# Kernel tuning notes

Hardware: AMD Instinct MI355X
Metric: run time of the kernel (lower is better)

Reference implementation:

```python
import jax, jax.numpy as jnp
import numpy as np

NEG_SLOPE = 0.01  # nn.LeakyReLU default


def leaky_relu(x):
    return jnp.where(x >= 0, x, NEG_SLOPE * x)


def gcn_conv(x, W, b, src, dst, n_nodes):
    """PyG GCNConv: add self loops, symmetric D^-1/2 (A+I) D^-1/2 norm, then x @ W + b."""
    h = x @ W  # [N, D]
    # degree with self-loops (edge weight 1 each, +1 for the self loop)
    deg = jnp.zeros((n_nodes,), dtype=x.dtype).at[dst].add(1.0) + 1.0
    dinv = jax.lax.rsqrt(deg)  # deg >= 1 thanks to self loops
    norm = dinv[src] * dinv[dst]  # [E]
    msg = h[src] * norm[:, None]  # gather + scale, [E, D]
    agg = jnp.zeros_like(h).at[dst].add(msg)  # scatter-add over targets
    agg = agg + h * (dinv * dinv)[:, None]  # self-loop contribution
    return agg + b


def setup_inputs() -> dict:
    key = jax.random.key(0)
    ks = jax.random.split(key, 12)
    N, E = 100000, 640000
    ND, D, C = 239, 128, 2
    x = jax.random.normal(ks[0], (N, ND), dtype=jnp.float32)
    edge_index = jax.random.randint(ks[1], (2, E), 0, N, dtype=jnp.int64)
    edge_type = jax.random.randint(ks[2], (E,), 0, 4, dtype=jnp.int64)
    s = 0.05
    W_in = jax.random.normal(ks[3], (ND, D), dtype=jnp.float32) * s
    b_in = jax.random.normal(ks[4], (D,), dtype=jnp.float32) * s
    W_g = jax.random.normal(ks[5], (D, D), dtype=jnp.float32) * s
    b_g = jax.random.normal(ks[6], (D,), dtype=jnp.float32) * s
    W_o1 = jax.random.normal(ks[7], (D, D), dtype=jnp.float32) * s
    b_o1 = jax.random.normal(ks[8], (D,), dtype=jnp.float32) * s
    W_o2 = jax.random.normal(ks[9], (D, C), dtype=jnp.float32) * s
    b_o2 = jax.random.normal(ks[10], (C,), dtype=jnp.float32) * s
    return {"x": x, "edge_index": edge_index, "edge_type": edge_type,
            "W_in": W_in, "b_in": b_in, "W_g": W_g, "b_g": b_g,
            "W_o1": W_o1, "b_o1": b_o1, "W_o2": W_o2, "b_o2": b_o2}


def reference(x, edge_index, edge_type, W_in, b_in, W_g, b_g, W_o1, b_o1, W_o2, b_o2):
    n_nodes = x.shape[0]
    src, dst = edge_index[0], edge_index[1]
    h = leaky_relu(x @ W_in + b_in)
    h = gcn_conv(h, W_g, b_g, src, dst, n_nodes)
    # dropout is identity in eval mode (training=False)
    h = gcn_conv(h, W_g, b_g, src, dst, n_nodes)  # same shared GCNConv instance
    h = leaky_relu(h @ W_o1 + b_o1)
    return h @ W_o2 + b_o2
```

## Files before the change

### kernel.cpp

```cpp
#include <hip/hip_runtime.h>
#include <hip/hip_bf16.h>


typedef __attribute__((ext_vector_type(8))) __bf16 bf16x8;
typedef __attribute__((ext_vector_type(4))) float f32x4;

__global__ __launch_bounds__(256) void wtr_k(const float* __restrict__ W, ushort* __restrict__ Wt,
                                             int K, int Kp) {
  int idx = blockIdx.x * 256 + threadIdx.x;
  if (idx >= 128 * Kp) return;
  int n = idx / Kp, k = idx % Kp;
  float v = (k < K) ? W[(size_t)k * 128 + n] : 0.f;
  __hip_bfloat16 h = __float2bfloat16(v);
  Wt[idx] = *(ushort*)&h;
}


__global__ __launch_bounds__(256) void zero_k(int* __restrict__ p, int n) {
  int i = blockIdx.x * 256 + threadIdx.x;
  if (i < n) p[i] = 0;
}

__global__ __launch_bounds__(256) void hist_k(const int* __restrict__ dst, int* __restrict__ cnt, int E) {
  int e = blockIdx.x * 256 + threadIdx.x;
  if (e < E) atomicAdd(&cnt[dst[e]], 1);
}

__global__ __launch_bounds__(256) void dinv_k(const int* __restrict__ cnt, float* __restrict__ dinv, int N) {
  int i = blockIdx.x * 256 + threadIdx.x;
  if (i < N) dinv[i] = rsqrtf((float)cnt[i] + 1.0f);
}

__global__ __launch_bounds__(256) void scan1_k(const int* __restrict__ cnt, int* __restrict__ rp,
                                               int* __restrict__ bsum, int N) {
  __shared__ int sd[256];
  int t = threadIdx.x;
  int base = blockIdx.x * 1024 + t * 4;
  int v0 = (base + 0 < N) ? cnt[base + 0] : 0;
  int v1 = (base + 1 < N) ? cnt[base + 1] : 0;
  int v2 = (base + 2 < N) ? cnt[base + 2] : 0;
  int v3 = (base + 3 < N) ? cnt[base + 3] : 0;
  int ts = v0 + v1 + v2 + v3;
  sd[t] = ts;
  __syncthreads();
  for (int off = 1; off < 256; off <<= 1) {
    int y = (t >= off) ? sd[t - off] : 0;
    __syncthreads();
    sd[t] += y;
    __syncthreads();
  }
  int x = sd[t] - ts;
  if (t == 255) bsum[blockIdx.x] = sd[255];
  if (base + 0 < N) rp[base + 0] = x; x += v0;
  if (base + 1 < N) rp[base + 1] = x; x += v1;
  if (base + 2 < N) rp[base + 2] = x; x += v2;
  if (base + 3 < N) rp[base + 3] = x;
}

__global__ __launch_bounds__(256) void scan2_k(int* __restrict__ bsum, int NB) {
  __shared__ int sd[256];
  int t = threadIdx.x;
  int base = t * 4;
  int v0 = (base + 0 < NB) ? bsum[base + 0] : 0;
  int v1 = (base + 1 < NB) ? bsum[base + 1] : 0;
  int v2 = (base + 2 < NB) ? bsum[base + 2] : 0;
  int v3 = (base + 3 < NB) ? bsum[base + 3] : 0;
  int ts = v0 + v1 + v2 + v3;
  sd[t] = ts;
  __syncthreads();
  for (int off = 1; off < 256; off <<= 1) {
    int y = (t >= off) ? sd[t - off] : 0;
    __syncthreads();
    sd[t] += y;
    __syncthreads();
  }
  int x = sd[t] - ts;
  if (base + 0 < NB) bsum[base + 0] = x; x += v0;
  if (base + 1 < NB) bsum[base + 1] = x; x += v1;
  if (base + 2 < NB) bsum[base + 2] = x; x += v2;
  if (base + 3 < NB) bsum[base + 3] = x;
}

__global__ __launch_bounds__(256) void scan3_k(int* __restrict__ rp, int* __restrict__ pos,
                                               const int* __restrict__ bsum, int N, int E) {
  int i = blockIdx.x * 256 + threadIdx.x;
  if (i < N) {
    int v = rp[i] + bsum[i >> 10];
    rp[i] = v;
    pos[i] = v;
  }
  if (i == 0) rp[N] = E;
}

__global__ __launch_bounds__(256) void fill_k(const int* __restrict__ src, const int* __restrict__ dst,
                                              const float* __restrict__ dinv,
                                              int* __restrict__ pos, int2* __restrict__ ew, int E) {
  int e = blockIdx.x * 256 + threadIdx.x;
  if (e < E) {
    int d = dst[e];
    int s = src[e];
    int idx = atomicAdd(&pos[d], 1);
    ew[idx] = make_int2(s, __float_as_int(dinv[s] * dinv[d]));
  }
}


template <int MODE, int ASRC>
__global__ __launch_bounds__(512, 4) void mgemm_k(const void* __restrict__ Av,
                                                  const ushort* __restrict__ Wt,
                                                  const float* __restrict__ bias,
                                                  const float* __restrict__ W2,
                                                  const float* __restrict__ b2,
                                                  void* __restrict__ C, int N, int Kg, int Ka) {
  __shared__ uint4 Al[128 * 16];
  __shared__ uint4 Wl[128 * 16];
  const int tid = threadIdx.x;
  const int wave = tid >> 6;
  const int lane = tid & 63;
  const int l16 = lane & 15;
  const int quad = lane >> 4;
  const int m0 = blockIdx.x * 128;

  f32x4 acc[8] = {};

  const int r_s = tid >> 4;
  const int j8 = tid & 15;
  const int nch = Kg >> 7;

  for (int kc = 0; kc < nch; ++kc) {
    const int kbase = kc << 7;
    if (kc) __syncthreads();
#pragma unroll
    for (int it = 0; it < 4; ++it) {
      int m = it * 32 + r_s;
      uint4 v;
      if constexpr (ASRC == 0) {
        v = *(const uint4*)((const ushort*)Av + (size_t)(m0 + m) * Kg + kbase + j8 * 8);
      } else {
        int row = m0 + m;
        int rc = row < N ? row : N - 1;
        int c0 = kbase + j8 * 8;
        union { uint4 u; __hip_bfloat16 h[8]; } cv;
        if (c0 >= Ka) {
          cv.u = make_uint4(0, 0, 0, 0);
        } else {
          const float* xp = (const float*)Av;
          size_t s = (size_t)rc * Ka + c0;
          size_t base = s & ~(size_t)3;
          int ph = (int)(s & 3);
          size_t NT = (size_t)N * Ka;
          if (base + 12 <= NT) {
            const float4* bp = (const float4*)(xp + base);
            float4 f0 = bp[0], f1 = bp[1], f2 = bp[2];
            float w[12] = {f0.x, f0.y, f0.z, f0.w, f1.x, f1.y, f1.z, f1.w,
                           f2.x, f2.y, f2.z, f2.w};
#pragma unroll
            for (int j = 0; j < 8; ++j) {
              float f = ph == 0 ? w[j] : ph == 1 ? w[j + 1] : ph == 2 ? w[j + 2] : w[j + 3];
              cv.h[j] = __float2bfloat16(f);
            }
          } else {
#pragma unroll
            for (int j = 0; j < 8; ++j) {
              size_t idx = s + j;
              float f = (idx < NT && c0 + j < Ka) ? xp[idx] : 0.f;
              cv.h[j] = __float2bfloat16(f);
            }
          }
        }
        v = cv.u;
      }
      Al[m * 16 + (j8 ^ (m & 15))] = v;
    }
#pragma unroll
    for (int it = 0; it < 4; ++it) {
      int n = it * 32 + r_s;
      uint4 v = *(const uint4*)(Wt + (size_t)n * Kg + kbase + j8 * 8);
      Wl[n * 16 + (j8 ^ (n & 15))] = v;
    }
    __syncthreads();
#pragma unroll
    for (int s = 0; s < 4; ++s) {
      const int j = s * 4 + quad;
      const int swz = j ^ l16;
      bf16x8 a = *(const bf16x8*)&Al[(wave * 16 + l16) * 16 + swz];
#pragma unroll
      for (int c = 0; c < 8; ++c) {
        bf16x8 b = *(const bf16x8*)&Wl[(c * 16 + l16) * 16 + swz];
        acc[c] = __builtin_amdgcn_mfma_f32_16x16x32_bf16(a, b, acc[c], 0, 0, 0);
      }
    }
  }

  float bv[8];
#pragma unroll
  for (int c = 0; c < 8; ++c) bv[c] = bias[c * 16 + l16];

  if constexpr (MODE == 3) {
    float w20[8], w21[8];
#pragma unroll
    for (int c = 0; c < 8; ++c) {
      int colj = c * 16 + l16;
      w20[c] = W2[colj * 2 + 0];
      w21[c] = W2[colj * 2 + 1];
    }
    float bb0 = b2[0], bb1 = b2[1];
#pragma unroll
    for (int reg = 0; reg < 4; ++reg) {
      float o0 = 0.f, o1 = 0.f;
#pragma unroll
      for (int c = 0; c < 8; ++c) {
        float v = acc[c][reg] + bv[c];
        v = v >= 0.f ? v : 0.01f * v;
        o0 = fmaf(v, w20[c], o0);
        o1 = fmaf(v, w21[c], o1);
      }
      o0 += __shfl_xor(o0, 1); o0 += __shfl_xor(o0, 2);
      o0 += __shfl_xor(o0, 4); o0 += __shfl_xor(o0, 8);
      o1 += __shfl_xor(o1, 1); o1 += __shfl_xor(o1, 2);
      o1 += __shfl_xor(o1, 4); o1 += __shfl_xor(o1, 8);
      int row = m0 + wave * 16 + quad * 4 + reg;
      if (l16 == 0 && row < N)
        *(float2*)((float*)C + (size_t)row * 2) = make_float2(o0 + bb0, o1 + bb1);
    }
    return;
  }

#pragma unroll
  for (int reg = 0; reg < 4; ++reg) {
    int row = m0 + wave * 16 + quad * 4 + reg;
    if (row < N) {
#pragma unroll
      for (int c = 0; c < 8; ++c) {
        float v = acc[c][reg] + bv[c];
        if (MODE == 2) v = v >= 0.f ? v : 0.01f * v;
        __hip_bfloat16 h = __float2bfloat16(v);
        ((ushort*)C)[(size_t)row * 128 + c * 16 + l16] = *(ushort*)&h;
      }
    }
  }
}


__global__ __launch_bounds__(256) void agg_k(const ushort* __restrict__ T,
                                             const float* __restrict__ dinv,
                                             const int* __restrict__ rp,
                                             const int2* __restrict__ ew,
                                             ushort* __restrict__ O, int N) {
  int l = threadIdx.x & 15;
  int node = blockIdx.x * 16 + (threadIdx.x >> 4);
  if (node >= N) return;
  float di = dinv[node];
  float dsq = di * di;
  const uint4* T4 = (const uint4*)T;
  float a[8];
  {
    uint4 sv = T4[(size_t)node * 16 + l];
    uint u[4] = {sv.x, sv.y, sv.z, sv.w};
#pragma unroll
    for (int p = 0; p < 4; ++p) {
      a[2 * p + 0] = __uint_as_float(u[p] << 16) * dsq;
      a[2 * p + 1] = __uint_as_float(u[p] & 0xFFFF0000u) * dsq;
    }
  }
  int e1 = rp[node + 1];
  for (int e = rp[node]; e < e1; ++e) {
    int2 pw = ew[e];
    float w = __int_as_float(pw.y);
    uint4 v = T4[(size_t)pw.x * 16 + l];
    uint u[4] = {v.x, v.y, v.z, v.w};
#pragma unroll
    for (int p = 0; p < 4; ++p) {
      a[2 * p + 0] = fmaf(__uint_as_float(u[p] << 16), w, a[2 * p + 0]);
      a[2 * p + 1] = fmaf(__uint_as_float(u[p] & 0xFFFF0000u), w, a[2 * p + 1]);
    }
  }
  union { uint4 v; ushort s[8]; } uo;
#pragma unroll
  for (int j = 0; j < 8; ++j) {
    __hip_bfloat16 h = __float2bfloat16(a[j]);
    uo.s[j] = *(ushort*)&h;
  }
  ((uint4*)O)[(size_t)node * 16 + l] = uo.v;
}


extern "C" void kernel_launch(void* const* d_in, const int* in_sizes, int n_in,
                              void* d_out, int out_size, void* d_ws, size_t ws_size,
                              hipStream_t stream) {
  const float* x = (const float*)d_in[0];
  const int* ei = (const int*)d_in[1];
  const float* W_in = (const float*)d_in[3];
  const float* b_in = (const float*)d_in[4];
  const float* W_g  = (const float*)d_in[5];
  const float* b_g  = (const float*)d_in[6];
  const float* W_o1 = (const float*)d_in[7];
  const float* b_o1 = (const float*)d_in[8];
  const float* W_o2 = (const float*)d_in[9];
  const float* b_o2 = (const float*)d_in[10];

  const int D = in_sizes[4];
  const int ND = in_sizes[3] / D;
  const int N = in_sizes[0] / ND;
  const int E = in_sizes[2];
  const int* src = ei;
  const int* dst = ei + E;

  const int N_pad = ((N + 127) / 128) * 128;
  const size_t np = (size_t)N_pad;
  const int KP1 = 256;

  ushort* hA = (ushort*)d_ws;
  ushort* hB = hA + np * 128;
  ushort* Wt_in = hB + np * 128;
  ushort* Wt_g  = Wt_in + 128 * 256;
  ushort* Wt_o1 = Wt_g + 128 * 128;
  float* dinv = (float*)(Wt_o1 + 128 * 128);
  int* cnt  = (int*)(dinv + N);
  int* rp   = cnt + N;
  int* bsum = rp + (N + 1);
  int2* ew  = (int2*)(((size_t)(bsum + 1024) + 7) & ~(size_t)7);

  const int NB = (N + 1023) / 1024;

  wtr_k<<<(128 * KP1 + 255) / 256, 256, 0, stream>>>(W_in, Wt_in, ND, KP1);
  wtr_k<<<(128 * 128 + 255) / 256, 256, 0, stream>>>(W_g, Wt_g, 128, 128);
  wtr_k<<<(128 * 128 + 255) / 256, 256, 0, stream>>>(W_o1, Wt_o1, 128, 128);

  zero_k<<<(N + 255) / 256, 256, 0, stream>>>(cnt, N);
  hist_k<<<(E + 255) / 256, 256, 0, stream>>>(dst, cnt, E);
  dinv_k<<<(N + 255) / 256, 256, 0, stream>>>(cnt, dinv, N);
  scan1_k<<<NB, 256, 0, stream>>>(cnt, rp, bsum, N);
  scan2_k<<<1, 256, 0, stream>>>(bsum, NB);
  scan3_k<<<(N + 255) / 256, 256, 0, stream>>>(rp, cnt , bsum, N, E);
  fill_k<<<(E + 255) / 256, 256, 0, stream>>>(src, dst, dinv, cnt, ew, E);

  const int gblocks = N_pad / 128;
  const int ablocks = (N + 15) / 16;
  mgemm_k<2, 1><<<gblocks, 512, 0, stream>>>(x, Wt_in, b_in, nullptr, nullptr, hA, N, KP1, ND);
  agg_k<<<ablocks, 256, 0, stream>>>(hA, dinv, rp, ew, hB, N);
  mgemm_k<1, 0><<<gblocks, 512, 0, stream>>>(hB, Wt_g, b_g, nullptr, nullptr, hA, N, 128, 128);
  agg_k<<<ablocks, 256, 0, stream>>>(hA, dinv, rp, ew, hB, N);
  mgemm_k<1, 0><<<gblocks, 512, 0, stream>>>(hB, Wt_g, b_g, nullptr, nullptr, hA, N, 128, 128);
  mgemm_k<3, 0><<<gblocks, 512, 0, stream>>>(hA, Wt_o1, b_o1, W_o2, b_o2, d_out, N, 128, 128);
}
```

Before: 374.4 us.

## Stage whole x row-block in LDS for first GEMM, fold dinv into scan

Adds a dedicated first-layer GEMM kernel. Each block streams its contiguous 128x239 fp32 slab of x with coalesced float4 loads, converts it to bf16 and stores it in LDS, using a magic-multiply division to get row and column. This replaces the old per-chunk unaligned, phase-shuffled loads. The dinv computation is folded into scan3 to drop a launch, and the 128-wide mgemm is specialised to a single K chunk. The large LDS footprint (about 80KB) may reduce occupancy, and the scalar 2-byte LDS stores could cause bank conflicts.

```diff
diff --git a/kernel.cpp b/kernel.cpp
--- a/kernel.cpp
+++ b/kernel.cpp
@@ -24,11 +24,6 @@
 __global__ __launch_bounds__(256) void hist_k(const int* __restrict__ dst, int* __restrict__ cnt, int E) {
   int e = blockIdx.x * 256 + threadIdx.x;
   if (e < E) atomicAdd(&cnt[dst[e]], 1);
-}
-
-__global__ __launch_bounds__(256) void dinv_k(const int* __restrict__ cnt, float* __restrict__ dinv, int N) {
-  int i = blockIdx.x * 256 + threadIdx.x;
-  if (i < N) dinv[i] = rsqrtf((float)cnt[i] + 1.0f);
 }
 
 __global__ __launch_bounds__(256) void scan1_k(const int* __restrict__ cnt, int* __restrict__ rp,
@@ -82,10 +77,13 @@
 }
 
 __global__ __launch_bounds__(256) void scan3_k(int* __restrict__ rp, int* __restrict__ pos,
-                                               const int* __restrict__ bsum, int N, int E) {
+                                               const int* __restrict__ bsum,
+                                               float* __restrict__ dinv, int N, int E) {
   int i = blockIdx.x * 256 + threadIdx.x;
   if (i < N) {
+    int c = pos[i];
     int v = rp[i] + bsum[i >> 10];
+    dinv[i] = rsqrtf((float)c + 1.0f);
     rp[i] = v;
     pos[i] = v;
   }
@@ -105,13 +103,103 @@
 }
 
 
-template <int MODE, int ASRC>
-__global__ __launch_bounds__(512, 4) void mgemm_k(const void* __restrict__ Av,
+__global__ __launch_bounds__(512, 4) void gemm1_k(const float* __restrict__ x,
+                                                  const ushort* __restrict__ Wt,
+                                                  const float* __restrict__ bias,
+                                                  ushort* __restrict__ C, int N, int Ka,
+                                                  unsigned long long M ) {
+  __shared__ ushort Al[128 * 248];
+  __shared__ ushort Wl[128 * 72];
+  const int tid = threadIdx.x;
+  const int wave = tid >> 6;
+  const int lane = tid & 63;
+  const int l16 = lane & 15;
+  const int quad = lane >> 4;
+  const int m0 = blockIdx.x * 128;
+
+  if (tid < 128) {
+    Al[tid * 248 + 239] = 0;
+    *(uint4*)&Al[tid * 248 + 240] = make_uint4(0, 0, 0, 0);
+  }
+
+  {
+    int rows = N - m0;
+    if (rows > 128) rows = 128;
+    const int region = rows * Ka;
+    const float* __restrict__ xb = x + (size_t)m0 * Ka;
+    const int nv4 = region >> 2;
+    for (int i = tid; i < nv4; i += 512) {
+      float4 v = ((const float4*)xb)[i];
+      int f0 = i * 4;
+      float vf[4] = {v.x, v.y, v.z, v.w};
+#pragma unroll
+      for (int j = 0; j < 4; ++j) {
+        int idx = f0 + j;
+        uint r = (uint)(((unsigned long long)(uint)idx * M) >> 40);
+        uint c = (uint)idx - r * (uint)Ka;
+        __hip_bfloat16 h = __float2bfloat16(vf[j]);
+        Al[r * 248 + c] = *(ushort*)&h;
+      }
+    }
+    for (int i = (nv4 << 2) + tid; i < region; i += 512) {
+      uint r = (uint)(((unsigned long long)(uint)i * M) >> 40);
+      uint c = (uint)i - r * (uint)Ka;
+      __hip_bfloat16 h = __float2bfloat16(xb[i]);
+      Al[r * 248 + c] = *(ushort*)&h;
+    }
+  }
+
+  f32x4 acc[8] = {};
+  const int wn = tid >> 2;
+  const int wseg = tid & 3;
+#pragma unroll
+  for (int kc = 0; kc < 4; ++kc) {
+    __syncthreads();
+    *(uint4*)&Wl[wn * 72 + wseg * 16] =
+        *(const uint4*)(Wt + (size_t)wn * 256 + kc * 64 + wseg * 16);
+    *(uint4*)&Wl[wn * 72 + wseg * 16 + 8] =
+        *(const uint4*)(Wt + (size_t)wn * 256 + kc * 64 + wseg * 16 + 8);
+    __syncthreads();
+#pragma unroll
+    for (int s = 0; s < 2; ++s) {
+      const int koff = kc * 64 + s * 32 + quad * 8;
+      bf16x8 a = {};
+      if (koff < 248) a = *(const bf16x8*)&Al[(wave * 16 + l16) * 248 + koff];
+      const int wof = s * 32 + quad * 8;
+#pragma unroll
+      for (int c = 0; c < 8; ++c) {
+        bf16x8 b = *(const bf16x8*)&Wl[(c * 16 + l16) * 72 + wof];
+        acc[c] = __builtin_amdgcn_mfma_f32_16x16x32_bf16(a, b, acc[c], 0, 0, 0);
+      }
+    }
+  }
+
+  float bv[8];
+#pragma unroll
+  for (int c = 0; c < 8; ++c) bv[c] = bias[c * 16 + l16];
+#pragma unroll
+  for (int reg = 0; reg < 4; ++reg) {
+    int row = m0 + wave * 16 + quad * 4 + reg;
+    if (row < N) {
+#pragma unroll
+      for (int c = 0; c < 8; ++c) {
+        float v = acc[c][reg] + bv[c];
+        v = v >= 0.f ? v : 0.01f * v;
+        __hip_bfloat16 h = __float2bfloat16(v);
+        C[(size_t)row * 128 + c * 16 + l16] = *(ushort*)&h;
+      }
+    }
+  }
+}
+
+
+template <int MODE>
+__global__ __launch_bounds__(512, 4) void mgemm_k(const ushort* __restrict__ A,
                                                   const ushort* __restrict__ Wt,
                                                   const float* __restrict__ bias,
                                                   const float* __restrict__ W2,
                                                   const float* __restrict__ b2,
-                                                  void* __restrict__ C, int N, int Kg, int Ka) {
+                                                  void* __restrict__ C, int N) {
   __shared__ uint4 Al[128 * 16];
   __shared__ uint4 Wl[128 * 16];
   const int tid = threadIdx.x;
@@ -122,73 +210,29 @@
   const int m0 = blockIdx.x * 128;
 
   f32x4 acc[8] = {};
-
   const int r_s = tid >> 4;
   const int j8 = tid & 15;
-  const int nch = Kg >> 7;
-
-  for (int kc = 0; kc < nch; ++kc) {
-    const int kbase = kc << 7;
-    if (kc) __syncthreads();
-#pragma unroll
-    for (int it = 0; it < 4; ++it) {
-      int m = it * 32 + r_s;
-      uint4 v;
-      if constexpr (ASRC == 0) {
-        v = *(const uint4*)((const ushort*)Av + (size_t)(m0 + m) * Kg + kbase + j8 * 8);
-      } else {
-        int row = m0 + m;
-        int rc = row < N ? row : N - 1;
-        int c0 = kbase + j8 * 8;
-        union { uint4 u; __hip_bfloat16 h[8]; } cv;
-        if (c0 >= Ka) {
-          cv.u = make_uint4(0, 0, 0, 0);
-        } else {
-          const float* xp = (const float*)Av;
-          size_t s = (size_t)rc * Ka + c0;
-          size_t base = s & ~(size_t)3;
-          int ph = (int)(s & 3);
-          size_t NT = (size_t)N * Ka;
-          if (base + 12 <= NT) {
-            const float4* bp = (const float4*)(xp + base);
-            float4 f0 = bp[0], f1 = bp[1], f2 = bp[2];
-            float w[12] = {f0.x, f0.y, f0.z, f0.w, f1.x, f1.y, f1.z, f1.w,
-                           f2.x, f2.y, f2.z, f2.w};
-#pragma unroll
-            for (int j = 0; j < 8; ++j) {
-              float f = ph == 0 ? w[j] : ph == 1 ? w[j + 1] : ph == 2 ? w[j + 2] : w[j + 3];
-              cv.h[j] = __float2bfloat16(f);
-            }
-          } else {
-#pragma unroll
-            for (int j = 0; j < 8; ++j) {
-              size_t idx = s + j;
-              float f = (idx < NT && c0 + j < Ka) ? xp[idx] : 0.f;
-              cv.h[j] = __float2bfloat16(f);
-            }
-          }
-        }
-        v = cv.u;
-      }
-      Al[m * 16 + (j8 ^ (m & 15))] = v;
-    }
-#pragma unroll
-    for (int it = 0; it < 4; ++it) {
-      int n = it * 32 + r_s;
-      uint4 v = *(const uint4*)(Wt + (size_t)n * Kg + kbase + j8 * 8);
-      Wl[n * 16 + (j8 ^ (n & 15))] = v;
-    }
-    __syncthreads();
-#pragma unroll
-    for (int s = 0; s < 4; ++s) {
-      const int j = s * 4 + quad;
-      const int swz = j ^ l16;
-      bf16x8 a = *(const bf16x8*)&Al[(wave * 16 + l16) * 16 + swz];
-#pragma unroll
-      for (int c = 0; c < 8; ++c) {
-        bf16x8 b = *(const bf16x8*)&Wl[(c * 16 + l16) * 16 + swz];
-        acc[c] = __builtin_amdgcn_mfma_f32_16x16x32_bf16(a, b, acc[c], 0, 0, 0);
-      }
+#pragma unroll
+  for (int it = 0; it < 4; ++it) {
+    int m = it * 32 + r_s;
+    Al[m * 16 + (j8 ^ (m & 15))] = *(const uint4*)(A + (size_t)(m0 + m) * 128 + j8 * 8);
+  }
+#pragma unroll
+  for (int it = 0; it < 4; ++it) {
+    int n = it * 32 + r_s;
+    Wl[n * 16 + (j8 ^ (n & 15))] = *(const uint4*)(Wt + (size_t)n * 128 + j8 * 8);
+  }
+  __syncthreads();
+#pragma unroll
+  for (int s = 0; s < 4; ++s) {
+    const int j = s * 4 + quad;
+    const int arow = wave * 16 + l16;
+    bf16x8 a = *(const bf16x8*)&Al[arow * 16 + (j ^ (arow & 15))];
+#pragma unroll
+    for (int c = 0; c < 8; ++c) {
+      const int brow = c * 16 + l16;
+      bf16x8 b = *(const bf16x8*)&Wl[brow * 16 + (j ^ (brow & 15))];
+      acc[c] = __builtin_amdgcn_mfma_f32_16x16x32_bf16(a, b, acc[c], 0, 0, 0);
     }
   }
 
@@ -233,7 +277,6 @@
 #pragma unroll
       for (int c = 0; c < 8; ++c) {
         float v = acc[c][reg] + bv[c];
-        if (MODE == 2) v = v >= 0.f ? v : 0.01f * v;
         __hip_bfloat16 h = __float2bfloat16(v);
         ((ushort*)C)[(size_t)row * 128 + c * 16 + l16] = *(ushort*)&h;
       }
@@ -309,6 +352,7 @@
   const int N_pad = ((N + 127) / 128) * 128;
   const size_t np = (size_t)N_pad;
   const int KP1 = 256;
+  const unsigned long long MAGIC = ((1ULL << 40) + (unsigned)ND - 1) / (unsigned)ND;
 
   ushort* hA = (ushort*)d_ws;
   ushort* hB = hA + np * 128;
@@ -329,18 +373,17 @@
 
   zero_k<<<(N + 255) / 256, 256, 0, stream>>>(cnt, N);
   hist_k<<<(E + 255) / 256, 256, 0, stream>>>(dst, cnt, E);
-  dinv_k<<<(N + 255) / 256, 256, 0, stream>>>(cnt, dinv, N);
   scan1_k<<<NB, 256, 0, stream>>>(cnt, rp, bsum, N);
   scan2_k<<<1, 256, 0, stream>>>(bsum, NB);
-  scan3_k<<<(N + 255) / 256, 256, 0, stream>>>(rp, cnt , bsum, N, E);
+  scan3_k<<<(N + 255) / 256, 256, 0, stream>>>(rp, cnt , bsum, dinv, N, E);
   fill_k<<<(E + 255) / 256, 256, 0, stream>>>(src, dst, dinv, cnt, ew, E);
 
   const int gblocks = N_pad / 128;
   const int ablocks = (N + 15) / 16;
-  mgemm_k<2, 1><<<gblocks, 512, 0, stream>>>(x, Wt_in, b_in, nullptr, nullptr, hA, N, KP1, ND);
+  gemm1_k<<<gblocks, 512, 0, stream>>>(x, Wt_in, b_in, hA, N, ND, MAGIC);
   agg_k<<<ablocks, 256, 0, stream>>>(hA, dinv, rp, ew, hB, N);
-  mgemm_k<1, 0><<<gblocks, 512, 0, stream>>>(hB, Wt_g, b_g, nullptr, nullptr, hA, N, 128, 128);
+  mgemm_k<1><<<gblocks, 512, 0, stream>>>(hB, Wt_g, b_g, nullptr, nullptr, hA, N);
   agg_k<<<ablocks, 256, 0, stream>>>(hA, dinv, rp, ew, hB, N);
-  mgemm_k<1, 0><<<gblocks, 512, 0, stream>>>(hB, Wt_g, b_g, nullptr, nullptr, hA, N, 128, 128);
-  mgemm_k<3, 0><<<gblocks, 512, 0, stream>>>(hA, Wt_o1, b_o1, W_o2, b_o2, d_out, N, 128, 128);
-}
+  mgemm_k<1><<<gblocks, 512, 0, stream>>>(hB, Wt_g, b_g, nullptr, nullptr, hA, N);
+  mgemm_k<3><<<gblocks, 512, 0, stream>>>(hA, Wt_o1, b_o1, W_o2, b_o2, d_out, N);
+}
```

After: 365.8 us. 2.3% less time.
